# Kernel tuning notes

Measured on AMD Instinct MI355X. Metric: run time of the kernel, lower is better.

## Reference

```python
import jax, jax.numpy as jnp
import numpy as np

NEG_SLOPE = 0.01  # torch F.leaky_relu default


def setup_inputs() -> dict:
    key = jax.random.key(0)
    k1, k2, k3, k4, k5 = jax.random.split(key, 5)
    n_nodes, n_edges, d = 50000, 1000000, 128
    return {
        "n_f": jax.random.normal(k1, (n_nodes, d), dtype=jnp.float32),
        "src_idx": jax.random.randint(k2, (n_edges,), 0, n_nodes, dtype=jnp.int32),
        "dst_idx": jax.random.randint(k3, (n_edges,), 0, n_nodes, dtype=jnp.int32),
        "W_edge": jax.random.normal(k4, (d, 2 * d), dtype=jnp.float32) * 0.05,  # [out_feat, in_feat]
        "W_attn": jax.random.normal(k5, (1, d), dtype=jnp.float32) * 0.05,      # [1, out_feat]
    }


def reference(n_f, src_idx, dst_idx, W_edge, W_attn):
    # gather src/dst node features per edge and concat: [E, 2*d]
    feat = jnp.concatenate([n_f[src_idx], n_f[dst_idx]], axis=1)
    # edge_fn (no bias) + ReLU: [E, out_feat]
    e_feat = jax.nn.relu(jnp.einsum("ei,oi->eo", feat, W_edge))
    # attn_fc (no bias) + leaky_relu: [E, 1]
    a_fact = jax.nn.leaky_relu(jnp.einsum("eo,ao->ea", e_feat, W_attn), NEG_SLOPE)
    return e_feat, a_fact
```

## Files before the change

kernel.cpp:

```cpp
#include <hip/hip_runtime.h>
#include <hip/hip_bf16.h>

typedef __attribute__((ext_vector_type(4))) float  f32x4;
typedef __attribute__((ext_vector_type(8))) short  bf16x8;
typedef __attribute__((ext_vector_type(4))) unsigned u32x4;
typedef __attribute__((ext_vector_type(2))) unsigned u32x2;

#define NEG_SLOPE 0.01f

__device__ __forceinline__ unsigned short f2bf(float f) {
    unsigned u = __builtin_bit_cast(unsigned, f);
    return (unsigned short)((u + 0x7FFFu + ((u >> 16) & 1u)) >> 16);
}
__device__ __forceinline__ unsigned pack2(float a, float b) {
    return (unsigned)f2bf(a) | ((unsigned)f2bf(b) << 16);
}

__global__ __launch_bounds__(256, 4)
void node_gemm_kernel(const float* __restrict__ n_f,
                      const float* __restrict__ W_edge,
                      unsigned short* __restrict__ uv,
                      int n_nodes)
{
    __shared__ short Ftile[64 * 128];

    const int tid  = threadIdx.x;
    const int lane = tid & 63;
    const int wave = tid >> 6;
    const int node_base = blockIdx.x * 64;

    #pragma unroll
    for (int it = 0; it < 4; ++it) {
        int r = it * 16 + (tid >> 4);
        int q = tid & 15;
        int gn = node_base + r;
        if (gn >= n_nodes) gn = n_nodes - 1;
        const float* p = n_f + (size_t)gn * 128 + q * 8;
        f32x4 v0 = *(const f32x4*)p;
        f32x4 v1 = *(const f32x4*)(p + 4);
        u32x4 u;
        u.x = pack2(v0.x, v0.y);
        u.y = pack2(v0.z, v0.w);
        u.z = pack2(v1.x, v1.y);
        u.w = pack2(v1.z, v1.w);
        int byteoff = (r * 256 + q * 16) ^ ((r & 7) << 4);
        *(u32x4*)((char*)Ftile + byteoff) = u;
    }

    const int an    = lane & 15;
    const int ak    = (lane >> 4) * 8;
    const int kofs  = (wave >= 2) ? 128 : 0;
    const int obase = (wave & 1) * 64;
    bf16x8 wfrag[4][4];
    #pragma unroll
    for (int nt = 0; nt < 4; ++nt) {
        #pragma unroll
        for (int kt = 0; kt < 4; ++kt) {
            const float* wp = W_edge + (size_t)(obase + nt * 16 + an) * 256 + kofs + kt * 32 + ak;
            f32x4 w0 = *(const f32x4*)wp;
            f32x4 w1 = *(const f32x4*)(wp + 4);
            bf16x8 f;
            f[0] = (short)f2bf(w0.x); f[1] = (short)f2bf(w0.y);
            f[2] = (short)f2bf(w0.z); f[3] = (short)f2bf(w0.w);
            f[4] = (short)f2bf(w1.x); f[5] = (short)f2bf(w1.y);
            f[6] = (short)f2bf(w1.z); f[7] = (short)f2bf(w1.w);
            wfrag[nt][kt] = f;
        }
    }

    __syncthreads();

    const int fe    = lane & 15;
    const int fkoff = (lane >> 4) * 16;
    #pragma unroll
    for (int mt = 0; mt < 4; ++mt) {
        f32x4 acc[4];
        #pragma unroll
        for (int nt = 0; nt < 4; ++nt) acc[nt] = (f32x4){0.f, 0.f, 0.f, 0.f};
        const int row = mt * 16 + fe;
        #pragma unroll
        for (int kt = 0; kt < 4; ++kt) {
            int byteoff = (row * 256 + kt * 64 + fkoff) ^ ((row & 7) << 4);
            bf16x8 ffrag = *(const bf16x8*)((const char*)Ftile + byteoff);
            #pragma unroll
            for (int nt = 0; nt < 4; ++nt)
                acc[nt] = __builtin_amdgcn_mfma_f32_16x16x32_bf16(wfrag[nt][kt], ffrag, acc[nt], 0, 0, 0);
        }
        int gn = node_base + mt * 16 + fe;
        if (gn < n_nodes) {
            unsigned short* op = uv + (size_t)gn * 256 + wave * 64 + (lane >> 4) * 4;
            #pragma unroll
            for (int nt = 0; nt < 4; ++nt) {
                u32x2 pk;
                pk.x = pack2(acc[nt][0], acc[nt][1]);
                pk.y = pack2(acc[nt][2], acc[nt][3]);
                *(u32x2*)(op + nt * 16) = pk;
            }
        }
    }
}

__device__ __forceinline__ void edge_compute_store(u32x2 du0, u32x2 du1,
                                                   u32x2 dv0, u32x2 dv1,
                                                   const f32x4& wa_lo, const f32x4& wa_hi,
                                                   float* __restrict__ e_out,
                                                   float* __restrict__ a_out,
                                                   int e, bool valid, int q)
{
    f32x4 r0, r1;
    #pragma unroll
    for (int j = 0; j < 2; ++j) {
        float ulo = __builtin_bit_cast(float, du0[j] << 16);
        float uhi = __builtin_bit_cast(float, du0[j] & 0xFFFF0000u);
        float vlo = __builtin_bit_cast(float, dv0[j] << 16);
        float vhi = __builtin_bit_cast(float, dv0[j] & 0xFFFF0000u);
        r0[2*j]   = fmaxf(ulo + vlo, 0.f);
        r0[2*j+1] = fmaxf(uhi + vhi, 0.f);

        float ulo1 = __builtin_bit_cast(float, du1[j] << 16);
        float uhi1 = __builtin_bit_cast(float, du1[j] & 0xFFFF0000u);
        float vlo1 = __builtin_bit_cast(float, dv1[j] << 16);
        float vhi1 = __builtin_bit_cast(float, dv1[j] & 0xFFFF0000u);
        r1[2*j]   = fmaxf(ulo1 + vlo1, 0.f);
        r1[2*j+1] = fmaxf(uhi1 + vhi1, 0.f);
    }

    if (valid) {
        float* ep = e_out + (size_t)e * 128;
        __builtin_nontemporal_store(r0, (f32x4*)(ep + q * 4));
        __builtin_nontemporal_store(r1, (f32x4*)(ep + 64 + q * 4));
    }

    float pd = r0[0]*wa_lo[0] + r0[1]*wa_lo[1] + r0[2]*wa_lo[2] + r0[3]*wa_lo[3]
             + r1[0]*wa_hi[0] + r1[1]*wa_hi[1] + r1[2]*wa_hi[2] + r1[3]*wa_hi[3];
    pd += __shfl_xor(pd, 1);
    pd += __shfl_xor(pd, 2);
    pd += __shfl_xor(pd, 4);
    pd += __shfl_xor(pd, 8);
    if (valid && q == 0) {
        float a = (pd > 0.f) ? pd : NEG_SLOPE * pd;
        __builtin_nontemporal_store(a, a_out + e);
    }
}

__global__ __launch_bounds__(256, 8)
void edge_apply_kernel(const int*   __restrict__ src_idx,
                       const int*   __restrict__ dst_idx,
                       const unsigned short* __restrict__ uv,
                       const float* __restrict__ W_attn,
                       float* __restrict__ e_out,
                       float* __restrict__ a_out,
                       int E)
{
    const int tid  = threadIdx.x;
    const int lane = tid & 63;
    const int wave = tid >> 6;
    const int q    = lane & 15;
    const int sub  = lane >> 4;

    const f32x4 wa_lo = *(const f32x4*)&W_attn[q * 4];
    const f32x4 wa_hi = *(const f32x4*)&W_attn[64 + q * 4];

    const int gw     = blockIdx.x * 4 + wave;
    const int stride = gridDim.x * 4 * 8;

    for (int e0 = gw * 8; e0 < E; e0 += stride) {
        int  eA = e0 + sub;
        int  eB = e0 + 4 + sub;
        bool vA = (eA < E);
        bool vB = (eB < E);
        int  esA = vA ? src_idx[eA] : 0;
        int  edA = vA ? dst_idx[eA] : 0;
        int  esB = vB ? src_idx[eB] : 0;
        int  edB = vB ? dst_idx[eB] : 0;

        const unsigned short* upA = uv + (size_t)esA * 256;
        const unsigned short* vpA = uv + (size_t)edA * 256 + 128;
        const unsigned short* upB = uv + (size_t)esB * 256;
        const unsigned short* vpB = uv + (size_t)edB * 256 + 128;
        u32x2 du0A = *(const u32x2*)(upA + q * 4);
        u32x2 du1A = *(const u32x2*)(upA + 64 + q * 4);
        u32x2 dv0A = *(const u32x2*)(vpA + q * 4);
        u32x2 dv1A = *(const u32x2*)(vpA + 64 + q * 4);
        u32x2 du0B = *(const u32x2*)(upB + q * 4);
        u32x2 du1B = *(const u32x2*)(upB + 64 + q * 4);
        u32x2 dv0B = *(const u32x2*)(vpB + q * 4);
        u32x2 dv1B = *(const u32x2*)(vpB + 64 + q * 4);

        edge_compute_store(du0A, du1A, dv0A, dv1A, wa_lo, wa_hi, e_out, a_out, eA, vA, q);
        edge_compute_store(du0B, du1B, dv0B, dv1B, wa_lo, wa_hi, e_out, a_out, eB, vB, q);
    }
}

#define ME 64
__global__ __launch_bounds__(256, 4)
void gat_edge_fused_kernel(const float* __restrict__ n_f,
                           const int*   __restrict__ src_idx,
                           const int*   __restrict__ dst_idx,
                           const float* __restrict__ W_edge,
                           const float* __restrict__ W_attn,
                           float* __restrict__ e_out,
                           float* __restrict__ a_out,
                           int E)
{
    __shared__ short Atile[ME * 256];
    __shared__ float a_acc[ME];

    const int tid  = threadIdx.x;
    const int lane = tid & 63;
    const int wave = tid >> 6;
    const int edge_base = blockIdx.x * ME;

    if (tid < ME) a_acc[tid] = 0.0f;

    #pragma unroll
    for (int it = 0; it < 8; ++it) {
        int pair = it * 16 + (tid >> 4);
        int e  = pair >> 1;
        int hf = pair & 1;
        int q  = tid & 15;
        int ge = edge_base + e;
        int idx = (ge < E) ? (hf ? dst_idx[ge] : src_idx[ge]) : 0;
        const float* p = n_f + (size_t)idx * 128 + q * 8;
        f32x4 v0 = *(const f32x4*)p;
        f32x4 v1 = *(const f32x4*)(p + 4);
        u32x4 u;
        u.x = pack2(v0.x, v0.y);
        u.y = pack2(v0.z, v0.w);
        u.z = pack2(v1.x, v1.y);
        u.w = pack2(v1.z, v1.w);
        int byteoff = (e * 512 + hf * 256 + q * 16) ^ ((e & 7) << 4);
        *(u32x4*)((char*)Atile + byteoff) = u;
    }

    const int an = lane & 15;
    const int ak = (lane >> 4) * 8;
    const int n0 = wave * 32;
    bf16x8 wfrag[2][8];
    #pragma unroll
    for (int nt = 0; nt < 2; ++nt) {
        #pragma unroll
        for (int kt = 0; kt < 8; ++kt) {
            const float* wp = W_edge + (size_t)(n0 + nt * 16 + an) * 256 + kt * 32 + ak;
            f32x4 w0 = *(const f32x4*)wp;
            f32x4 w1 = *(const f32x4*)(wp + 4);
            bf16x8 f;
            f[0] = (short)f2bf(w0.x); f[1] = (short)f2bf(w0.y);
            f[2] = (short)f2bf(w0.z); f[3] = (short)f2bf(w0.w);
            f[4] = (short)f2bf(w1.x); f[5] = (short)f2bf(w1.y);
            f[6] = (short)f2bf(w1.z); f[7] = (short)f2bf(w1.w);
            wfrag[nt][kt] = f;
        }
    }
    f32x4 wa[2];
    wa[0] = *(const f32x4*)&W_attn[n0 + (lane >> 4) * 4];
    wa[1] = *(const f32x4*)&W_attn[n0 + 16 + (lane >> 4) * 4];

    __syncthreads();

    const int fe    = lane & 15;
    const int fkoff = (lane >> 4) * 16;
    #pragma unroll
    for (int et = 0; et < 4; ++et) {
        const int erow = et * 16 + fe;
        f32x4 acc0 = {0.f, 0.f, 0.f, 0.f};
        f32x4 acc1 = {0.f, 0.f, 0.f, 0.f};
        #pragma unroll
        for (int kt = 0; kt < 8; ++kt) {
            int byteoff = (erow * 512 + kt * 64 + fkoff) ^ ((erow & 7) << 4);
            bf16x8 ffrag = *(const bf16x8*)((const char*)Atile + byteoff);
            acc0 = __builtin_amdgcn_mfma_f32_16x16x32_bf16(wfrag[0][kt], ffrag, acc0, 0, 0, 0);
            acc1 = __builtin_amdgcn_mfma_f32_16x16x32_bf16(wfrag[1][kt], ffrag, acc1, 0, 0, 0);
        }
        const int ge = edge_base + et * 16 + fe;
        f32x4 c0, c1;
        #pragma unroll
        for (int j = 0; j < 4; ++j) {
            c0[j] = fmaxf(acc0[j], 0.f);
            c1[j] = fmaxf(acc1[j], 0.f);
        }
        if (ge < E) {
            float* ep = e_out + (size_t)ge * 128 + n0 + (lane >> 4) * 4;
            *(f32x4*)ep        = c0;
            *(f32x4*)(ep + 16) = c1;
        }
        float pdot = c0[0]*wa[0][0] + c0[1]*wa[0][1] + c0[2]*wa[0][2] + c0[3]*wa[0][3]
                   + c1[0]*wa[1][0] + c1[1]*wa[1][1] + c1[2]*wa[1][2] + c1[3]*wa[1][3];
        pdot += __shfl_xor(pdot, 16);
        pdot += __shfl_xor(pdot, 32);
        if (lane < 16) atomicAdd(&a_acc[et * 16 + lane], pdot);
    }

    __syncthreads();
    if (tid < ME) {
        int ge = edge_base + tid;
        if (ge < E) {
            float a = a_acc[tid];
            a_out[ge] = (a > 0.f) ? a : NEG_SLOPE * a;
        }
    }
}

extern "C" void kernel_launch(void* const* d_in, const int* in_sizes, int n_in,
                              void* d_out, int out_size, void* d_ws, size_t ws_size,
                              hipStream_t stream) {
    const float* n_f     = (const float*)d_in[0];
    const int*   src_idx = (const int*)d_in[1];
    const int*   dst_idx = (const int*)d_in[2];
    const float* W_edge  = (const float*)d_in[3];
    const float* W_attn  = (const float*)d_in[4];
    const int E       = in_sizes[1];
    const int n_nodes = in_sizes[0] / 128;

    float* e_out = (float*)d_out;
    float* a_out = e_out + (size_t)E * 128;

    const size_t uv_bytes = (size_t)n_nodes * 256 * sizeof(unsigned short);
    if (ws_size >= uv_bytes) {
        unsigned short* uv = (unsigned short*)d_ws;
        int nb1 = (n_nodes + 63) / 64;
        node_gemm_kernel<<<nb1, 256, 0, stream>>>(n_f, W_edge, uv, n_nodes);
        edge_apply_kernel<<<2048, 256, 0, stream>>>(src_idx, dst_idx, uv, W_attn,
                                                    e_out, a_out, E);
    } else {
        int nblocks = (E + ME - 1) / ME;
        gat_edge_fused_kernel<<<nblocks, 256, 0, stream>>>(n_f, src_idx, dst_idx,
                                                           W_edge, W_attn, e_out, a_out, E);
    }
}
```

Baseline: 185.1 us.

## Counting-sort edges by source node before the gather-apply pass

Adds a histogram of source indices, folded into the node GEMM launch as extra blocks, then a single-block prefix scan and an atomic scatter that builds source-sorted edge lists. The edge apply kernel then walks the sorted order, so source-row gathers of the bf16 projection table hit cache more often. The cost is three extra passes over the edge indices, a serial one-block scan, and scattered writes of e_feat rows because output rows now follow the permuted order. The attention output store also changes from nontemporal to a normal store.

```diff
diff --git a/kernel.cpp b/kernel.cpp
--- a/kernel.cpp
+++ b/kernel.cpp
@@ -7,6 +7,7 @@
 typedef __attribute__((ext_vector_type(2))) unsigned u32x2;
 
 #define NEG_SLOPE 0.01f
+#define NBH 512
 
 __device__ __forceinline__ unsigned short f2bf(float f) {
     unsigned u = __builtin_bit_cast(unsigned, f);
@@ -17,14 +18,24 @@
 }
 
 __global__ __launch_bounds__(256, 4)
-void node_gemm_kernel(const float* __restrict__ n_f,
-                      const float* __restrict__ W_edge,
-                      unsigned short* __restrict__ uv,
-                      int n_nodes)
+void node_gemm_hist_kernel(const float* __restrict__ n_f,
+                           const float* __restrict__ W_edge,
+                           unsigned short* __restrict__ uv,
+                           int n_nodes,
+                           const int* __restrict__ src_idx, int E,
+                           int* __restrict__ hist, int nb1)
 {
     __shared__ short Ftile[64 * 128];
 
-    const int tid  = threadIdx.x;
+    const int tid = threadIdx.x;
+
+    if ((int)blockIdx.x >= nb1) {
+        int b = blockIdx.x - nb1;
+        for (int e = b * 256 + tid; e < E; e += NBH * 256)
+            atomicAdd(&hist[src_idx[e]], 1);
+        return;
+    }
+
     const int lane = tid & 63;
     const int wave = tid >> 6;
     const int node_base = blockIdx.x * 64;
@@ -100,6 +111,64 @@
     }
 }
 
+__global__ __launch_bounds__(1024, 1)
+void scan_kernel(const int* __restrict__ hist, int* __restrict__ offs, int n)
+{
+    __shared__ int wtot[16];
+    __shared__ int carry_s;
+    const int tid  = threadIdx.x;
+    const int lane = tid & 63;
+    const int wid  = tid >> 6;
+    if (tid == 0) carry_s = 0;
+    __syncthreads();
+
+    for (int base = 0; base < n; base += 1024) {
+        int i = base + tid;
+        int x = (i < n) ? hist[i] : 0;
+        int v = x;
+        #pragma unroll
+        for (int d = 1; d < 64; d <<= 1) {
+            int t = __shfl_up(v, d);
+            if (lane >= d) v += t;
+        }
+        if (lane == 63) wtot[wid] = v;
+        __syncthreads();
+        if (wid == 0) {
+            int wv = (lane < 16) ? wtot[lane] : 0;
+            #pragma unroll
+            for (int d = 1; d < 16; d <<= 1) {
+                int t = __shfl_up(wv, d);
+                if (lane >= d) wv += t;
+            }
+            if (lane < 16) wtot[lane] = wv;
+        }
+        __syncthreads();
+        int wbase = (wid == 0) ? 0 : wtot[wid - 1];
+        int carry = carry_s;
+        if (i < n) offs[i] = carry + wbase + v - x;
+        int chunk_total = wtot[15];
+        __syncthreads();
+        if (tid == 0) carry_s = carry + chunk_total;
+        __syncthreads();
+    }
+}
+
+__global__ __launch_bounds__(256, 8)
+void scatter_kernel(const int* __restrict__ src_idx,
+                    const int* __restrict__ dst_idx,
+                    int* __restrict__ offs,
+                    int* __restrict__ ss, int* __restrict__ sd, int* __restrict__ se,
+                    int E)
+{
+    for (int e = blockIdx.x * 256 + threadIdx.x; e < E; e += gridDim.x * 256) {
+        int s = src_idx[e];
+        int pos = atomicAdd(&offs[s], 1);
+        ss[pos] = s;
+        sd[pos] = dst_idx[e];
+        se[pos] = e;
+    }
+}
+
 __device__ __forceinline__ void edge_compute_store(u32x2 du0, u32x2 du1,
                                                    u32x2 dv0, u32x2 dv1,
                                                    const f32x4& wa_lo, const f32x4& wa_hi,
@@ -139,7 +208,59 @@
     pd += __shfl_xor(pd, 8);
     if (valid && q == 0) {
         float a = (pd > 0.f) ? pd : NEG_SLOPE * pd;
-        __builtin_nontemporal_store(a, a_out + e);
+        a_out[e] = a;
+    }
+}
+
+__global__ __launch_bounds__(256, 8)
+void edge_apply_sorted_kernel(const int* __restrict__ ss,
+                              const int* __restrict__ sd,
+                              const int* __restrict__ se,
+                              const unsigned short* __restrict__ uv,
+                              const float* __restrict__ W_attn,
+                              float* __restrict__ e_out,
+                              float* __restrict__ a_out,
+                              int E)
+{
+    const int tid  = threadIdx.x;
+    const int lane = tid & 63;
+    const int wave = tid >> 6;
+    const int q    = lane & 15;
+    const int sub  = lane >> 4;
+
+    const f32x4 wa_lo = *(const f32x4*)&W_attn[q * 4];
+    const f32x4 wa_hi = *(const f32x4*)&W_attn[64 + q * 4];
+
+    const int gw     = blockIdx.x * 4 + wave;
+    const int stride = gridDim.x * 4 * 8;
+
+    for (int e0 = gw * 8; e0 < E; e0 += stride) {
+        int  iA = e0 + sub;
+        int  iB = e0 + 4 + sub;
+        bool vA = (iA < E);
+        bool vB = (iB < E);
+        int  sA = vA ? ss[iA] : 0;
+        int  dA = vA ? sd[iA] : 0;
+        int  eA = vA ? se[iA] : 0;
+        int  sB = vB ? ss[iB] : 0;
+        int  dB = vB ? sd[iB] : 0;
+        int  eB = vB ? se[iB] : 0;
+
+        const unsigned short* upA = uv + (size_t)sA * 256;
+        const unsigned short* vpA = uv + (size_t)dA * 256 + 128;
+        const unsigned short* upB = uv + (size_t)sB * 256;
+        const unsigned short* vpB = uv + (size_t)dB * 256 + 128;
+        u32x2 du0A = *(const u32x2*)(upA + q * 4);
+        u32x2 du1A = *(const u32x2*)(upA + 64 + q * 4);
+        u32x2 dv0A = *(const u32x2*)(vpA + q * 4);
+        u32x2 dv1A = *(const u32x2*)(vpA + 64 + q * 4);
+        u32x2 du0B = *(const u32x2*)(upB + q * 4);
+        u32x2 du1B = *(const u32x2*)(upB + 64 + q * 4);
+        u32x2 dv0B = *(const u32x2*)(vpB + q * 4);
+        u32x2 dv1B = *(const u32x2*)(vpB + 64 + q * 4);
+
+        edge_compute_store(du0A, du1A, dv0A, dv1A, wa_lo, wa_hi, e_out, a_out, eA, vA, q);
+        edge_compute_store(du0B, du1B, dv0B, dv1B, wa_lo, wa_hi, e_out, a_out, eB, vB, q);
     }
 }
 
@@ -315,11 +436,37 @@
     float* e_out = (float*)d_out;
     float* a_out = e_out + (size_t)E * 128;
 
-    const size_t uv_bytes = (size_t)n_nodes * 256 * sizeof(unsigned short);
-    if (ws_size >= uv_bytes) {
-        unsigned short* uv = (unsigned short*)d_ws;
+    const size_t uv_b    = (size_t)n_nodes * 256 * sizeof(unsigned short);
+    const size_t off_uv  = 0;
+    const size_t off_ss  = (off_uv + uv_b + 15) & ~(size_t)15;
+    const size_t off_sd  = (off_ss + (size_t)E * 4 + 15) & ~(size_t)15;
+    const size_t off_se  = (off_sd + (size_t)E * 4 + 15) & ~(size_t)15;
+    const size_t off_hi  = (off_se + (size_t)E * 4 + 15) & ~(size_t)15;
+    const size_t off_of  = (off_hi + (size_t)n_nodes * 4 + 15) & ~(size_t)15;
+    const size_t total   = off_of + (size_t)n_nodes * 4;
+
+    char* ws = (char*)d_ws;
+    if (ws_size >= total) {
+        unsigned short* uv = (unsigned short*)(ws + off_uv);
+        int* ss   = (int*)(ws + off_ss);
+        int* sd   = (int*)(ws + off_sd);
+        int* se   = (int*)(ws + off_se);
+        int* hist = (int*)(ws + off_hi);
+        int* offs = (int*)(ws + off_of);
+
         int nb1 = (n_nodes + 63) / 64;
-        node_gemm_kernel<<<nb1, 256, 0, stream>>>(n_f, W_edge, uv, n_nodes);
+        hipMemsetAsync(hist, 0, (size_t)n_nodes * 4, stream);
+        node_gemm_hist_kernel<<<nb1 + NBH, 256, 0, stream>>>(n_f, W_edge, uv, n_nodes,
+                                                             src_idx, E, hist, nb1);
+        scan_kernel<<<1, 1024, 0, stream>>>(hist, offs, n_nodes);
+        scatter_kernel<<<1024, 256, 0, stream>>>(src_idx, dst_idx, offs, ss, sd, se, E);
+        edge_apply_sorted_kernel<<<2048, 256, 0, stream>>>(ss, sd, se, uv, W_attn,
+                                                           e_out, a_out, E);
+    } else if (ws_size >= uv_b) {
+        unsigned short* uv = (unsigned short*)ws;
+        int nb1 = (n_nodes + 63) / 64;
+        node_gemm_hist_kernel<<<nb1, 256, 0, stream>>>(n_f, W_edge, uv, n_nodes,
+                                                       src_idx, E, (int*)nullptr, nb1);
         edge_apply_kernel<<<2048, 256, 0, stream>>>(src_idx, dst_idx, uv, W_attn,
                                                     e_out, a_out, E);
     } else {
```

Result: slower. 295.9 us (+59.8%).
